# Performance work log

Hardware: AMD Instinct MI355X
Metric: run time of the kernel (lower is better)

## Reference

```python
import jax, jax.numpy as jnp
import numpy as np

KS = 5   # kernel_size per pseudo-dim
DIM = 3  # pseudo-coordinate dim
S = 2 ** DIM  # contributing B-spline (degree 1) basis combos per edge


def spline_conv(x, edge_index, pseudo, weight, root, bias, kernel_size=KS, dim=DIM):
    """Degree-1 open B-spline conv (PyG SplineConv, aggr='mean', root_weight, bias)."""
    src, dst = edge_index[0], edge_index[1]
    N, Cin = x.shape
    Ktot, _, Cout = weight.shape  # Ktot = kernel_size**dim
    v = pseudo * (kernel_size - 1)          # open spline: [E, dim]
    lo = jnp.floor(v)
    frac = v - lo
    lo = lo.astype(jnp.int32)
    bits = ((jnp.arange(S)[:, None] >> jnp.arange(dim)[None, :]) & 1)  # [S, dim]
    b = jnp.where(bits[None] == 1, frac[:, None, :], 1.0 - frac[:, None, :])  # [E,S,dim]
    basis = jnp.prod(b, axis=-1)                                            # [E,S]
    idx = jnp.clip(lo[:, None, :] + bits[None], 0, kernel_size - 1)          # [E,S,dim]
    mult = (kernel_size ** jnp.arange(dim)).astype(jnp.int32)
    kidx = jnp.sum(idx * mult, axis=-1)                                      # [E,S]
    xj = x[src]                                                              # [E,Cin]
    contrib = (basis[:, :, None] * xj[:, None, :]).reshape(-1, Cin)          # [E*S,Cin]
    seg = (dst[:, None] * Ktot + kidx).reshape(-1)                           # [E*S]
    # A[n,k,i] = sum of basis-weighted source features per (target node, kernel idx)
    A = jax.ops.segment_sum(contrib, seg, num_segments=N * Ktot).reshape(N, Ktot, Cin)
    deg = jax.ops.segment_sum(jnp.ones_like(dst, jnp.float32), dst, num_segments=N)
    out = jnp.einsum('nki,kio->no', A, weight) / jnp.maximum(deg, 1.0)[:, None]
    return out + x @ root + bias


def knn_interp(x, pos_x, pos_y, batch_x, batch_y, k):
    # squared dists via gemm: [Ny, Nx]
    d2 = (jnp.sum(pos_y * pos_y, -1)[:, None]
          + jnp.sum(pos_x * pos_x, -1)[None, :]
          - 2.0 * pos_y @ pos_x.T)
    d2 = jnp.where(batch_y[:, None] != batch_x[None, :], 1e10, d2)
    neg, idx = jax.lax.top_k(-d2, k)                  # [Ny, k]
    w = 1.0 / jnp.maximum(-neg, 1e-16)                # inverse-squared-distance weights
    w = jax.lax.stop_gradient(w)                      # PyG computes weights under no_grad
    num = jnp.einsum('yk,ykc->yc', w, x[idx])
    return num / jnp.sum(w, -1, keepdims=True)


def setup_inputs() -> dict:
    key = jax.random.key(0)
    ks = jax.random.split(key, 8)
    Nx, Ny, E, Cin, Cout = 4096, 16384, 65536, 64, 64
    return {
        'x': jax.random.normal(ks[0], (Nx, Cin), jnp.float32),
        'pos_x': jax.random.normal(ks[1], (Nx, DIM), jnp.float32),
        'pos_y': jax.random.normal(ks[2], (Ny, DIM), jnp.float32),
        'edge_index': jax.random.randint(ks[3], (2, E), 0, Nx, jnp.int32),
        'edge_attr': jax.random.uniform(ks[4], (E, DIM), jnp.float32),
        'batch_x': jnp.zeros((Nx,), jnp.int32),
        'batch_y': jnp.zeros((Ny,), jnp.int32),
        'weight': jax.random.normal(ks[5], (KS ** DIM, Cin, Cout), jnp.float32) * 0.05,
        'root': jax.random.normal(ks[6], (Cin, Cout), jnp.float32) * 0.05,
        'bias': jnp.zeros((Cout,), jnp.float32),
        'k': 3,
    }


def reference(x, pos_x, pos_y, edge_index, edge_attr, batch_x, batch_y, weight, root, bias, k):
    h = jax.nn.elu(spline_conv(x, edge_index, edge_attr, weight, root, bias))
    return knn_interp(h, pos_x, pos_y, batch_x, batch_y, k)
```

## Files before the change

kernel.cpp:

```cpp
#include <hip/hip_runtime.h>
#include <stdint.h>

#define WAVE 64
#define CIN 64
#define COUT 64
#define KS 5
#define KTOT 125
#define NSPLIT 16
#define KB4 32
#define BM 1e5f

typedef __attribute__((ext_vector_type(8))) short short8v;
typedef __attribute__((ext_vector_type(4))) float f32x4;

__device__ inline unsigned long long wmin64(unsigned long long v) {
#pragma unroll
  for (int o = 32; o >= 1; o >>= 1) {
    unsigned long long u = __shfl_xor(v, o, 64);
    v = (u < v) ? u : v;
  }
  return v;
}

__device__ inline unsigned f32_orderable(float f) {
  unsigned fb = __float_as_uint(f);
  return (fb & 0x80000000u) ? ~fb : (fb | 0x80000000u);
}
__device__ inline float f32_unorderable(unsigned u) {
  unsigned fb = (u & 0x80000000u) ? (u & 0x7fffffffu) : ~u;
  return __uint_as_float(fb);
}

__device__ inline unsigned short f2bf(float f) {
  unsigned u = __float_as_uint(f);
  unsigned r = (u + 0x7fffu + ((u >> 16) & 1u)) >> 16;
  return (unsigned short)r;
}
__device__ inline float bf2f(unsigned short v) {
  return __uint_as_float(((unsigned)v) << 16);
}

__device__ __forceinline__ float qnorm4(float q0, float q1, float q2, float q3) {
  return fmaf(q0, q0, fmaf(q1, q1, fmaf(q2, q2, q3 * q3)));
}
__device__ __forceinline__ float dist2(float q0, float q1, float q2, float q3,
                                       float py2t, float4 c, float c3) {
  float dot = fmaf(q0, c.x, fmaf(q1, c.y, fmaf(q2, c.z, q3 * c3)));
  return fmaf(-2.f, dot, py2t + c.w);
}

__device__ inline void edge_basis(const float* __restrict__ pseudo, int e,
                                  float bas[8], int kidx[8]) {
  float v0 = pseudo[e * 3 + 0] * (float)(KS - 1);
  float v1 = pseudo[e * 3 + 1] * (float)(KS - 1);
  float v2 = pseudo[e * 3 + 2] * (float)(KS - 1);
  float l0 = floorf(v0), l1 = floorf(v1), l2 = floorf(v2);
  float f0 = v0 - l0, f1 = v1 - l1, f2 = v2 - l2;
  int i0 = (int)l0, i1 = (int)l1, i2 = (int)l2;
#pragma unroll
  for (int s = 0; s < 8; s++) {
    int b0 = s & 1, b1 = (s >> 1) & 1, b2 = (s >> 2) & 1;
    float bb = (b0 ? f0 : 1.f - f0) * (b1 ? f1 : 1.f - f1) * (b2 ? f2 : 1.f - f2);
    int j0 = i0 + b0; j0 = j0 < 0 ? 0 : (j0 > KS - 1 ? KS - 1 : j0);
    int j1 = i1 + b1; j1 = j1 < 0 ? 0 : (j1 > KS - 1 ? KS - 1 : j1);
    int j2 = i2 + b2; j2 = j2 < 0 ? 0 : (j2 > KS - 1 ? KS - 1 : j2);
    bas[s] = bb;
    kidx[s] = j0 + KS * j1 + KS * KS * j2;
  }
}

__global__ __launch_bounds__(256) void pre_kernel(
    const float* __restrict__ x, unsigned short* __restrict__ xbf, int n4,
    const float* __restrict__ Wf, unsigned short* __restrict__ wbf,
    const float* __restrict__ pos_x, const int* __restrict__ batch_x,
    float4* __restrict__ pxp4, float* __restrict__ pxb, int Nx_,
    float* __restrict__ zbase, int nz4, int nb_zero, int nb_cvtx) {
  __shared__ float L[64][68];
  int bid = blockIdx.x;
  int tid = threadIdx.x;

  if (bid < nb_zero) {
    int i = bid * 256 + tid;
    if (i < nz4) *(float4*)&zbase[i * 4] = make_float4(0.f, 0.f, 0.f, 0.f);
    return;
  }
  bid -= nb_zero;
  if (bid < nb_cvtx) {
    int i = bid * 256 + tid;
    if (i >= n4) return;
    float4 v = *(const float4*)&x[i * 4];
    *(ushort4*)&xbf[i * 4] =
        make_ushort4(f2bf(v.x), f2bf(v.y), f2bf(v.z), f2bf(v.w));
    return;
  }
  bid -= nb_cvtx;
  if (bid < KTOT) {
    int k = bid;
    {
      int i = tid >> 2, o0 = (tid & 3) * 16;
      const float* src = Wf + (size_t)k * 4096 + i * 64 + o0;
      float4 a = *(const float4*)src;
      float4 b = *(const float4*)(src + 4);
      float4 c = *(const float4*)(src + 8);
      float4 d = *(const float4*)(src + 12);
      *(float4*)&L[i][o0 + 0] = a;
      *(float4*)&L[i][o0 + 4] = b;
      *(float4*)&L[i][o0 + 8] = c;
      *(float4*)&L[i][o0 + 12] = d;
    }
    __syncthreads();
    int o = tid >> 2, i0 = (tid & 3) * 16;
    unsigned short* dst = wbf + (size_t)k * 4096 + o * 64 + i0;
#pragma unroll
    for (int g = 0; g < 4; g++) {
      *(ushort4*)&dst[g * 4] =
          make_ushort4(f2bf(L[i0 + g * 4 + 0][o]), f2bf(L[i0 + g * 4 + 1][o]),
                       f2bf(L[i0 + g * 4 + 2][o]), f2bf(L[i0 + g * 4 + 3][o]));
    }
    return;
  }
  bid -= KTOT;
  {
    int t = bid * 256 + tid;
    if (t >= Nx_) return;
    float a0 = pos_x[t * 3 + 0], a1 = pos_x[t * 3 + 1], a2 = pos_x[t * 3 + 2];
    float bm = (float)batch_x[t] * BM;
    pxp4[t] = make_float4(a0, a1, a2, qnorm4(a0, a1, a2, bm));
    pxb[t] = bm;
  }
}

__global__ __launch_bounds__(256) void phaseQ_kernel(
    const float4* __restrict__ pxp4, const float* __restrict__ pxb,
    const float* __restrict__ pos_y, const int* __restrict__ batch_y,
    const int* __restrict__ kptr, float* __restrict__ vpart,
    int Ny_, int csize, int nb_knn, int nqb,
    const unsigned short* __restrict__ xbf,
    const unsigned short* __restrict__ wbf,
    unsigned short* __restrict__ xw, int Nx_, int nxb) {
  __shared__ char smem[8192];
  int bid = blockIdx.x;
  int tid = threadIdx.x;

  if (bid < nb_knn) {
    if (*kptr > 3) return;
    float4* lc = (float4*)smem;
    float* lb = (float*)(smem + 4096);
    const float FINF = __uint_as_float(0x7f800000u);

    int split = bid / nqb;
    int qy = (bid % nqb) * 256 + tid;
    int base0 = split * csize;

    int qc = qy < Ny_ ? qy : Ny_ - 1;
    float q0 = pos_y[qc * 3 + 0], q1 = pos_y[qc * 3 + 1], q2 = pos_y[qc * 3 + 2];
    float q3 = (float)batch_y[qc] * BM;
    float py2t = qnorm4(q0, q1, q2, q3);

    float b0 = FINF, b1 = FINF, b2 = FINF;

    for (int tb = 0; tb < csize; tb += 256) {
      int t = base0 + tb + tid;
      float4 cv;
      float cb;
      if (t < Nx_) {
        cv = pxp4[t];
        cb = pxb[t];
      } else {
        cv = make_float4(0.f, 0.f, 0.f, FINF);
        cb = 0.f;
      }
      __syncthreads();
      lc[tid] = cv;
      lb[tid] = cb;
      __syncthreads();

#pragma unroll 4
      for (int j = 0; j < 256; j++) {
        float d2 = dist2(q0, q1, q2, q3, py2t, lc[j], lb[j]);
        float n0 = fminf(d2, b0);
        float n1 = fminf(fmaxf(d2, b0), b1);
        float n2 = fminf(fmaxf(d2, b1), b2);
        b0 = n0; b1 = n1; b2 = n2;
      }
    }

    if (qy < Ny_) {
      float* vp = vpart + ((size_t)split * Ny_ + qy) * 3;
      vp[0] = b0;
      vp[1] = b1;
      vp[2] = b2;
    }
    return;
  }

  {
    int b = bid - nb_knn;
    int n0 = (b % nxb) * 64;
    int kg4 = b / nxb;
    unsigned short(*Sm)[64] = (unsigned short(*)[64])smem;

    int w = tid >> 6, lane = tid & 63;
    int lr = lane & 15, kg = lane >> 4;
    int rA = n0 + w * 16 + lr;
    if (rA >= Nx_) rA = Nx_ - 1;

    short8v a0 = *(const short8v*)&xbf[(size_t)rA * CIN + kg * 8];
    short8v a1 = *(const short8v*)&xbf[(size_t)rA * CIN + 32 + kg * 8];

    for (int kk4 = 0; kk4 < 4; kk4++) {
      int k = kg4 * 4 + kk4;
      if (k >= KTOT) break;
      const unsigned short* wb = wbf + (size_t)k * 4096;
#pragma unroll
      for (int ct = 0; ct < 4; ct++) {
        int col = ct * 16 + lr;
        short8v b0 = *(const short8v*)&wb[col * 64 + kg * 8];
        short8v b1 = *(const short8v*)&wb[col * 64 + 32 + kg * 8];
        f32x4 c = {0.f, 0.f, 0.f, 0.f};
        c = __builtin_amdgcn_mfma_f32_16x16x32_bf16(a0, b0, c, 0, 0, 0);
        c = __builtin_amdgcn_mfma_f32_16x16x32_bf16(a1, b1, c, 0, 0, 0);
#pragma unroll
        for (int r = 0; r < 4; r++) {
          Sm[w * 16 + kg * 4 + r][ct * 16 + lr] = f2bf(c[r]);
        }
      }
      __syncthreads();

#pragma unroll
      for (int round = 0; round < 2; round++) {
        int rr = (tid >> 3) + round * 32;
        int ch = (tid & 7) * 8;
        int grow = n0 + rr;
        if (grow < Nx_) {
          uint4 v = *(const uint4*)&Sm[rr][ch];
          *(uint4*)&xw[((size_t)k * Nx_ + grow) * COUT + ch] = v;
        }
      }
      __syncthreads();
    }
  }
}

__global__ __launch_bounds__(256) void phaseR_kernel(
    const float* __restrict__ vpart,
    const float4* __restrict__ pxp4, const float* __restrict__ pxb,
    const float* __restrict__ pos_y, const int* __restrict__ batch_y,
    const int* __restrict__ kptr, unsigned long long* __restrict__ part,
    int Ny_, int csize, int nb_knn, int nqb,
    const int* __restrict__ ei, const float* __restrict__ pseudo,
    const unsigned short* __restrict__ xw, float* __restrict__ acc,
    float* __restrict__ deg, int E_, int Nx_) {
  __shared__ char smem[5120];
  int bid = blockIdx.x;
  int tid = threadIdx.x;

  if (bid < nb_knn) {
    int kk = *kptr;
    if (kk > 3) return;
    kk = kk < 1 ? 1 : kk;
    float4* lc = (float4*)smem;
    float* lb = (float*)(smem + 4096);
    const float FINF = __uint_as_float(0x7f800000u);

    int split = bid / nqb;
    int qy = (bid % nqb) * 256 + tid;
    int base0 = split * csize;

    int qc = qy < Ny_ ? qy : Ny_ - 1;
    float q0 = pos_y[qc * 3 + 0], q1 = pos_y[qc * 3 + 1], q2 = pos_y[qc * 3 + 2];
    float q3 = (float)batch_y[qc] * BM;
    float py2t = qnorm4(q0, q1, q2, q3);

    float t0v = FINF, t1v = FINF, t2v = FINF;
#pragma unroll
    for (int s = 0; s < NSPLIT; s++) {
      const float* vp = vpart + ((size_t)s * Ny_ + qc) * 3;
#pragma unroll
      for (int r = 0; r < 3; r++) {
        float v = vp[r];
        float n0 = fminf(v, t0v);
        float n1 = fminf(fmaxf(v, t0v), t1v);
        float n2 = fminf(fmaxf(v, t1v), t2v);
        t0v = n0; t1v = n1; t2v = n2;
      }
    }
    float thr = kk == 1 ? t0v : (kk == 2 ? t1v : t2v);

    unsigned long long k0 = ~0ull, k1 = ~0ull, k2 = ~0ull;

    for (int tb = 0; tb < csize; tb += 256) {
      int t = base0 + tb + tid;
      float4 cv;
      float cb;
      if (t < Nx_) {
        cv = pxp4[t];
        cb = pxb[t];
      } else {
        cv = make_float4(0.f, 0.f, 0.f, FINF);
        cb = 0.f;
      }
      __syncthreads();
      lc[tid] = cv;
      lb[tid] = cb;
      __syncthreads();

#pragma unroll 4
      for (int j = 0; j < 256; j++) {
        float d2 = dist2(q0, q1, q2, q3, py2t, lc[j], lb[j]);
        if (d2 <= thr) {
          unsigned long long key =
              (((unsigned long long)f32_orderable(d2)) << 32) |
              (unsigned)(base0 + tb + j);
          {
            bool lt = key < k0;
            unsigned long long nv = lt ? key : k0;
            unsigned long long xv = lt ? k0 : key;
            k0 = nv; key = xv;
          }
          {
            bool lt = key < k1;
            unsigned long long nv = lt ? key : k1;
            unsigned long long xv = lt ? k1 : key;
            k1 = nv; key = xv;
          }
          k2 = key < k2 ? key : k2;
        }
      }
    }

    if (qy < Ny_) {
      unsigned long long* pp = part + ((size_t)split * Ny_ + qy) * 3;
      pp[0] = k0;
      pp[1] = k1;
      pp[2] = k2;
    }
    return;
  }

  {
    int b = bid - nb_knn;
    int lane = tid & 63;
    int e = (int)(((size_t)b * 256 + tid) >> 6);
    if (e >= E_) return;
    int src = ei[e];
    int dst = ei[E_ + e];
    float bas[8];
    int kidx[8];
    edge_basis(pseudo, e, bas, kidx);

    float y = 0.f;
#pragma unroll
    for (int s = 0; s < 8; s++) {
      y = fmaf(bas[s], bf2f(xw[((size_t)kidx[s] * Nx_ + src) * COUT + lane]), y);
    }
    atomicAdd(&acc[(size_t)dst * COUT + lane], y);
    if (lane == 0) atomicAdd(&deg[dst], 1.f);
  }
}

__global__ void node_finish_kernel(const float* __restrict__ x,
                                   const float* __restrict__ root,
                                   const float* __restrict__ bias,
                                   const float* __restrict__ acc,
                                   const float* __restrict__ deg,
                                   float* __restrict__ h, int Nx_) {
  int lane = threadIdx.x & 63;
  int n = (int)((blockIdx.x * blockDim.x + threadIdx.x) >> 6);
  if (n >= Nx_) return;
  float xs = x[(size_t)n * CIN + lane];
  float r = 0.f;
#pragma unroll 4
  for (int i = 0; i < CIN; i++) {
    float xv = __shfl(xs, i, 64);
    r = fmaf(xv, root[i * COUT + lane], r);
  }
  float d = deg[n];
  d = d > 1.f ? d : 1.f;
  float o = acc[(size_t)n * COUT + lane] / d + r + bias[lane];
  h[(size_t)n * COUT + lane] = (o > 0.f) ? o : expm1f(o);
}

__global__ void knn_merge_kernel(const unsigned long long* __restrict__ part,
                                 const float* __restrict__ h,
                                 const int* __restrict__ kptr,
                                 float* __restrict__ out, int Nx_, int Ny_) {
  int kk = *kptr;
  if (kk > 3) return;
  kk = kk < 1 ? 1 : kk;
  int lane = threadIdx.x & 63;
  int qy = (int)((blockIdx.x * blockDim.x + threadIdx.x) >> 6);
  if (qy >= Ny_) return;

  unsigned long long key = ~0ull;
  if (lane < 3 * NSPLIT) {
    key = part[((size_t)(lane / 3) * Ny_ + qy) * 3 + (lane % 3)];
  }

  float num = 0.f, den = 0.f;
  for (int i = 0; i < kk; i++) {
    unsigned long long m = wmin64(key);
    if (key == m) key = ~0ull;
    unsigned u = (unsigned)(m >> 32);
    int idx = (int)(m & 0xffffffffu);
    idx = (idx < 0 || idx >= Nx_) ? 0 : idx;
    float d2 = f32_unorderable(u);
    float w = 1.f / fmaxf(d2, 1e-16f);
    num = fmaf(w, h[(size_t)idx * COUT + lane], num);
    den += w;
  }
  out[(size_t)qy * COUT + lane] = num / den;
}

__global__ void knn_generic_kernel(const float* __restrict__ h,
                                   const float4* __restrict__ pxp4,
                                   const float* __restrict__ pxb,
                                   const float* __restrict__ pos_y,
                                   const int* __restrict__ batch_y,
                                   const int* __restrict__ kptr,
                                   float* __restrict__ out,
                                   int Nx_, int Ny_) {
  int kk = *kptr;
  if (kk <= 3) return;
  kk = kk > 8 ? 8 : kk;
  int lane = threadIdx.x & 63;
  int yy = (int)((blockIdx.x * blockDim.x + threadIdx.x) >> 6);
  if (yy >= Ny_) return;

  float q0 = pos_y[yy * 3 + 0], q1 = pos_y[yy * 3 + 1], q2 = pos_y[yy * 3 + 2];
  float q3 = (float)batch_y[yy] * BM;
  float py2t = qnorm4(q0, q1, q2, q3);

  unsigned long long best[8];
#pragma unroll
  for (int j = 0; j < 8; j++) best[j] = ~0ull;

  for (int t0 = 0; t0 < Nx_; t0 += 64) {
    int t = t0 + lane;
    unsigned long long key = ~0ull;
    if (t < Nx_) {
      float d2 = dist2(q0, q1, q2, q3, py2t, pxp4[t], pxb[t]);
      key = (((unsigned long long)f32_orderable(d2)) << 32) | (unsigned)t;
    }
    if (key < best[7]) {
#pragma unroll
      for (int j = 0; j < 8; j++) {
        unsigned long long mn = key < best[j] ? key : best[j];
        unsigned long long mx = key < best[j] ? best[j] : key;
        best[j] = mn;
        key = mx;
      }
    }
  }

  float num = 0.f, den = 0.f;
  for (int j = 0; j < kk; j++) {
    unsigned long long m = wmin64(best[0]);
    if (best[0] == m) {
#pragma unroll
      for (int t = 0; t < 7; t++) best[t] = best[t + 1];
      best[7] = ~0ull;
    }
    unsigned u = (unsigned)(m >> 32);
    int idx = (int)(m & 0xffffffffu);
    idx = (idx < 0 || idx >= Nx_) ? 0 : idx;
    float d2 = f32_unorderable(u);
    float w = 1.f / fmaxf(d2, 1e-16f);
    num = fmaf(w, h[(size_t)idx * COUT + lane], num);
    den += w;
  }
  out[(size_t)yy * COUT + lane] = num / den;
}

extern "C" void kernel_launch(void* const* d_in, const int* in_sizes, int n_in,
                              void* d_out, int out_size, void* d_ws, size_t ws_size,
                              hipStream_t stream) {
  const float* x = (const float*)d_in[0];
  const float* pos_x = (const float*)d_in[1];
  const float* pos_y = (const float*)d_in[2];
  const int* eidx = (const int*)d_in[3];
  const float* pseudo = (const float*)d_in[4];
  const int* batch_x = (const int*)d_in[5];
  const int* batch_y = (const int*)d_in[6];
  const float* W = (const float*)d_in[7];
  const float* root = (const float*)d_in[8];
  const float* bias = (const float*)d_in[9];
  const int* kptr = (const int*)d_in[10];

  int Nx = in_sizes[0] / CIN;
  int Ny = in_sizes[2] / 3;
  int E = in_sizes[3] / 2;

  int csize = ((Nx + NSPLIT - 1) / NSPLIT + 255) & ~255;
  if (csize < 256) csize = 256;

  float* acc = (float*)d_ws;
  float* deg = acc + (size_t)Nx * COUT;
  float* h = deg + Nx;
  float4* pxp4 = (float4*)(h + (size_t)Nx * COUT);
  float* pxb = (float*)(pxp4 + Nx);
  unsigned short* xbf = (unsigned short*)(pxb + Nx);
  unsigned short* wbf = xbf + (size_t)Nx * CIN;
  unsigned short* xw = wbf + (size_t)KTOT * CIN * COUT;
  float* vpart = (float*)(xw + (size_t)Nx * KTOT * COUT);
  uintptr_t paddr = (uintptr_t)(vpart + (size_t)NSPLIT * Ny * 3);
  paddr = (paddr + 7) & ~(uintptr_t)7;
  unsigned long long* part = (unsigned long long*)paddr;

  float* out = (float*)d_out;

  int n4 = Nx * CIN / 4;
  int nb_cvtx = (n4 + 255) / 256;
  int nb_pack = (Nx + 255) / 256;
  int nz4 = (Nx * COUT + Nx) / 4;
  int nb_zero = (nz4 + 255) / 256;
  int nqb = (Ny + 255) / 256;
  int nb_knn = nqb * NSPLIT;
  int nxb = (Nx + 63) / 64;
  int nkg4 = (KTOT + 3) / 4;
  int nb_xw = nxb * nkg4;
  int nb_edge = (int)(((size_t)E * WAVE + 255) / 256);

  pre_kernel<<<nb_zero + nb_cvtx + KTOT + nb_pack, 256, 0, stream>>>(
      x, xbf, n4, W, wbf, pos_x, batch_x, pxp4, pxb, Nx, acc, nz4, nb_zero,
      nb_cvtx);

  phaseQ_kernel<<<nb_knn + nb_xw, 256, 0, stream>>>(
      pxp4, pxb, pos_y, batch_y, kptr, vpart, Ny, csize, nb_knn, nqb,
      xbf, wbf, xw, Nx, nxb);

  phaseR_kernel<<<nb_knn + nb_edge, 256, 0, stream>>>(
      vpart, pxp4, pxb, pos_y, batch_y, kptr, part, Ny, csize, nb_knn, nqb,
      eidx, pseudo, xw, acc, deg, E, Nx);

  {
    int blocks = (Nx * WAVE + 255) / 256;
    node_finish_kernel<<<blocks, 256, 0, stream>>>(x, root, bias, acc, deg, h, Nx);
  }
  {
    int blocks = (Ny * WAVE + 255) / 256;
    knn_merge_kernel<<<blocks, 256, 0, stream>>>(part, h, kptr, out, Nx, Ny);
    knn_generic_kernel<<<blocks, 256, 0, stream>>>(h, pxp4, pxb, pos_y, batch_y,
                                                   kptr, out, Nx, Ny);
  }
}
```

Before: 102.9 us.

## Merge generic kNN into merge kernel, widen xw k-groups, add nontemporal xw accesses

Folds the k>3 generic kNN path into the merge kernel so one launch serves both cases, removing a launch that did nothing for k=3. Each xw-precompute block now covers 8 kernel indices instead of 4, so there are half as many blocks, each doing more work while reusing the same A fragments. Stores to and gathers from the xw buffer now use nontemporal hints to reduce cache pollution. Risks: fewer blocks lowers parallelism in phaseQ, and nontemporal loads on a gathered buffer could lose L2 reuse.

```diff
diff --git a/kernel.cpp b/kernel.cpp
--- a/kernel.cpp
+++ b/kernel.cpp
@@ -7,11 +7,11 @@
 #define KS 5
 #define KTOT 125
 #define NSPLIT 16
-#define KB4 32
 #define BM 1e5f
 
 typedef __attribute__((ext_vector_type(8))) short short8v;
 typedef __attribute__((ext_vector_type(4))) float f32x4;
+typedef __attribute__((ext_vector_type(4))) unsigned uint4v;
 
 __device__ inline unsigned long long wmin64(unsigned long long v) {
 #pragma unroll
@@ -197,7 +197,7 @@
   {
     int b = bid - nb_knn;
     int n0 = (b % nxb) * 64;
-    int kg4 = b / nxb;
+    int kg8 = b / nxb;
     unsigned short(*Sm)[64] = (unsigned short(*)[64])smem;
 
     int w = tid >> 6, lane = tid & 63;
@@ -208,8 +208,8 @@
     short8v a0 = *(const short8v*)&xbf[(size_t)rA * CIN + kg * 8];
     short8v a1 = *(const short8v*)&xbf[(size_t)rA * CIN + 32 + kg * 8];
 
-    for (int kk4 = 0; kk4 < 4; kk4++) {
-      int k = kg4 * 4 + kk4;
+    for (int kk8 = 0; kk8 < 8; kk8++) {
+      int k = kg8 * 8 + kk8;
       if (k >= KTOT) break;
       const unsigned short* wb = wbf + (size_t)k * 4096;
 #pragma unroll
@@ -233,8 +233,9 @@
         int ch = (tid & 7) * 8;
         int grow = n0 + rr;
         if (grow < Nx_) {
-          uint4 v = *(const uint4*)&Sm[rr][ch];
-          *(uint4*)&xw[((size_t)k * Nx_ + grow) * COUT + ch] = v;
+          uint4v v = *(const uint4v*)&Sm[rr][ch];
+          __builtin_nontemporal_store(
+              v, (uint4v*)&xw[((size_t)k * Nx_ + grow) * COUT + ch]);
         }
       }
       __syncthreads();
@@ -352,7 +353,9 @@
     float y = 0.f;
 #pragma unroll
     for (int s = 0; s < 8; s++) {
-      y = fmaf(bas[s], bf2f(xw[((size_t)kidx[s] * Nx_ + src) * COUT + lane]), y);
+      unsigned short v = __builtin_nontemporal_load(
+          &xw[((size_t)kidx[s] * Nx_ + src) * COUT + lane]);
+      y = fmaf(bas[s], bf2f(v), y);
     }
     atomicAdd(&acc[(size_t)dst * COUT + lane], y);
     if (lane == 0) atomicAdd(&deg[dst], 1.f);
@@ -383,93 +386,82 @@
 
 __global__ void knn_merge_kernel(const unsigned long long* __restrict__ part,
                                  const float* __restrict__ h,
+                                 const float4* __restrict__ pxp4,
+                                 const float* __restrict__ pxb,
+                                 const float* __restrict__ pos_y,
+                                 const int* __restrict__ batch_y,
                                  const int* __restrict__ kptr,
                                  float* __restrict__ out, int Nx_, int Ny_) {
   int kk = *kptr;
-  if (kk > 3) return;
-  kk = kk < 1 ? 1 : kk;
   int lane = threadIdx.x & 63;
   int qy = (int)((blockIdx.x * blockDim.x + threadIdx.x) >> 6);
   if (qy >= Ny_) return;
 
-  unsigned long long key = ~0ull;
-  if (lane < 3 * NSPLIT) {
-    key = part[((size_t)(lane / 3) * Ny_ + qy) * 3 + (lane % 3)];
-  }
-
   float num = 0.f, den = 0.f;
-  for (int i = 0; i < kk; i++) {
-    unsigned long long m = wmin64(key);
-    if (key == m) key = ~0ull;
-    unsigned u = (unsigned)(m >> 32);
-    int idx = (int)(m & 0xffffffffu);
-    idx = (idx < 0 || idx >= Nx_) ? 0 : idx;
-    float d2 = f32_unorderable(u);
-    float w = 1.f / fmaxf(d2, 1e-16f);
-    num = fmaf(w, h[(size_t)idx * COUT + lane], num);
-    den += w;
-  }
+
+  if (kk <= 3) {
+    kk = kk < 1 ? 1 : kk;
+    unsigned long long key = ~0ull;
+    if (lane < 3 * NSPLIT) {
+      key = part[((size_t)(lane / 3) * Ny_ + qy) * 3 + (lane % 3)];
+    }
+    for (int i = 0; i < kk; i++) {
+      unsigned long long m = wmin64(key);
+      if (key == m) key = ~0ull;
+      unsigned u = (unsigned)(m >> 32);
+      int idx = (int)(m & 0xffffffffu);
+      idx = (idx < 0 || idx >= Nx_) ? 0 : idx;
+      float d2 = f32_unorderable(u);
+      float w = 1.f / fmaxf(d2, 1e-16f);
+      num = fmaf(w, h[(size_t)idx * COUT + lane], num);
+      den += w;
+    }
+  } else {
+    kk = kk > 8 ? 8 : kk;
+    float q0 = pos_y[qy * 3 + 0], q1 = pos_y[qy * 3 + 1], q2 = pos_y[qy * 3 + 2];
+    float q3 = (float)batch_y[qy] * BM;
+    float py2t = qnorm4(q0, q1, q2, q3);
+
+    unsigned long long best[8];
+#pragma unroll
+    for (int j = 0; j < 8; j++) best[j] = ~0ull;
+
+    for (int t0 = 0; t0 < Nx_; t0 += 64) {
+      int t = t0 + lane;
+      unsigned long long key = ~0ull;
+      if (t < Nx_) {
+        float d2 = dist2(q0, q1, q2, q3, py2t, pxp4[t], pxb[t]);
+        key = (((unsigned long long)f32_orderable(d2)) << 32) | (unsigned)t;
+      }
+      if (key < best[7]) {
+#pragma unroll
+        for (int j = 0; j < 8; j++) {
+          unsigned long long mn = key < best[j] ? key : best[j];
+          unsigned long long mx = key < best[j] ? best[j] : key;
+          best[j] = mn;
+          key = mx;
+        }
+      }
+    }
+
+    for (int j = 0; j < kk; j++) {
+      unsigned long long m = wmin64(best[0]);
+      if (best[0] == m) {
+#pragma unroll
+        for (int t = 0; t < 7; t++) best[t] = best[t + 1];
+        best[7] = ~0ull;
+      }
+      unsigned u = (unsigned)(m >> 32);
+      int idx = (int)(m & 0xffffffffu);
+      idx = (idx < 0 || idx >= Nx_) ? 0 : idx;
+      float d2 = f32_unorderable(u);
+      float w = 1.f / fmaxf(d2, 1e-16f);
+      num = fmaf(w, h[(size_t)idx * COUT + lane], num);
+      den += w;
+    }
+  }
+
   out[(size_t)qy * COUT + lane] = num / den;
-}
-
-__global__ void knn_generic_kernel(const float* __restrict__ h,
-                                   const float4* __restrict__ pxp4,
-                                   const float* __restrict__ pxb,
-                                   const float* __restrict__ pos_y,
-                                   const int* __restrict__ batch_y,
-                                   const int* __restrict__ kptr,
-                                   float* __restrict__ out,
-                                   int Nx_, int Ny_) {
-  int kk = *kptr;
-  if (kk <= 3) return;
-  kk = kk > 8 ? 8 : kk;
-  int lane = threadIdx.x & 63;
-  int yy = (int)((blockIdx.x * blockDim.x + threadIdx.x) >> 6);
-  if (yy >= Ny_) return;
-
-  float q0 = pos_y[yy * 3 + 0], q1 = pos_y[yy * 3 + 1], q2 = pos_y[yy * 3 + 2];
-  float q3 = (float)batch_y[yy] * BM;
-  float py2t = qnorm4(q0, q1, q2, q3);
-
-  unsigned long long best[8];
-#pragma unroll
-  for (int j = 0; j < 8; j++) best[j] = ~0ull;
-
-  for (int t0 = 0; t0 < Nx_; t0 += 64) {
-    int t = t0 + lane;
-    unsigned long long key = ~0ull;
-    if (t < Nx_) {
-      float d2 = dist2(q0, q1, q2, q3, py2t, pxp4[t], pxb[t]);
-      key = (((unsigned long long)f32_orderable(d2)) << 32) | (unsigned)t;
-    }
-    if (key < best[7]) {
-#pragma unroll
-      for (int j = 0; j < 8; j++) {
-        unsigned long long mn = key < best[j] ? key : best[j];
-        unsigned long long mx = key < best[j] ? best[j] : key;
-        best[j] = mn;
-        key = mx;
-      }
-    }
-  }
-
-  float num = 0.f, den = 0.f;
-  for (int j = 0; j < kk; j++) {
-    unsigned long long m = wmin64(best[0]);
-    if (best[0] == m) {
-#pragma unroll
-      for (int t = 0; t < 7; t++) best[t] = best[t + 1];
-      best[7] = ~0ull;
-    }
-    unsigned u = (unsigned)(m >> 32);
-    int idx = (int)(m & 0xffffffffu);
-    idx = (idx < 0 || idx >= Nx_) ? 0 : idx;
-    float d2 = f32_unorderable(u);
-    float w = 1.f / fmaxf(d2, 1e-16f);
-    num = fmaf(w, h[(size_t)idx * COUT + lane], num);
-    den += w;
-  }
-  out[(size_t)yy * COUT + lane] = num / den;
 }
 
 extern "C" void kernel_launch(void* const* d_in, const int* in_sizes, int n_in,
@@ -517,8 +509,8 @@
   int nqb = (Ny + 255) / 256;
   int nb_knn = nqb * NSPLIT;
   int nxb = (Nx + 63) / 64;
-  int nkg4 = (KTOT + 3) / 4;
-  int nb_xw = nxb * nkg4;
+  int nkg8 = (KTOT + 7) / 8;
+  int nb_xw = nxb * nkg8;
   int nb_edge = (int)(((size_t)E * WAVE + 255) / 256);
 
   pre_kernel<<<nb_zero + nb_cvtx + KTOT + nb_pack, 256, 0, stream>>>(
@@ -539,8 +531,7 @@
   }
   {
     int blocks = (Ny * WAVE + 255) / 256;
-    knn_merge_kernel<<<blocks, 256, 0, stream>>>(part, h, kptr, out, Nx, Ny);
-    knn_generic_kernel<<<blocks, 256, 0, stream>>>(h, pxp4, pxb, pos_y, batch_y,
-                                                   kptr, out, Nx, Ny);
-  }
-}
+    knn_merge_kernel<<<blocks, 256, 0, stream>>>(part, h, pxp4, pxb, pos_y,
+                                                 batch_y, kptr, out, Nx, Ny);
+  }
+}
```

Measured after the change: 98.73 us (median of 2 runs). -4.0%, faster.
